# Optimization experiments

Hardware: AMD Instinct MI355X
Metric: run time of the kernel (lower is better)

## Reference

```python
import jax, jax.numpy as jnp
import numpy as np


def setup_inputs() -> dict:
    key = jax.random.key(0)
    k1, k2 = jax.random.split(key)
    B, C, H, W = 16, 512, 64, 64
    x_training = jax.random.normal(k1, (B, C, H, W), dtype=jnp.float32)
    x_pre = jax.random.normal(k2, (B, C, H, W), dtype=jnp.float32)
    return {"x_training": x_training, "x_pre": x_pre}


def reference(x_training, x_pre):
    B, C, H, W = x_training.shape
    q = x_pre.reshape(B, C, H * W)        # proj_query: B x C x N
    kv = x_training.reshape(B, C, H * W)  # proj_key/value: B x C x N
    # energy[b,c,d] = <q[b,c,:], kv[b,d,:]>  -> B x C x C
    energy = jnp.einsum('bcn,bdn->bcd', q, kv)
    # max-subtract trick (note: max - energy, not energy - max)
    energy_new = jnp.max(energy, axis=-1, keepdims=True) - energy
    attention = jax.nn.softmax(energy_new, axis=-1)  # B x C x C
    out = jnp.einsum('bcd,bdn->bcn', attention, kv).reshape(B, C, H, W)
    # final softmax over last (width) axis of the 4D map
    return jax.nn.softmax(out, axis=-1)
```

## Files before the change

### kernel.cpp

```cpp
#include <hip/hip_runtime.h>
#include <hip/hip_bf16.h>
#include <math.h>

#define CCH  512
#define NTOK 4096
#define NB   16
#define KSPL 2048
#define LDA  40

typedef __attribute__((ext_vector_type(8))) short s8v;
typedef __attribute__((ext_vector_type(4))) float f4v;
typedef unsigned short u16;

__device__ __forceinline__ void split2(float2 f, ushort2& hi, ushort2& lo) {
    __hip_bfloat162 h = __float22bfloat162_rn(f);
    float2 hf = __bfloat1622float2(h);
    __hip_bfloat162 l = __float22bfloat162_rn(make_float2(f.x - hf.x, f.y - hf.y));
    hi = *reinterpret_cast<ushort2*>(&h);
    lo = *reinterpret_cast<ushort2*>(&l);
}
__device__ __forceinline__ u16 bfrne(float x) {
    __hip_bfloat16 h = __float2bfloat16(x);
    return *reinterpret_cast<u16*>(&h);
}

__global__ __launch_bounds__(256, 2)
void energy_mfma(const float* __restrict__ q, const float* __restrict__ kv,
                 float* __restrict__ E) {
    __shared__ short Ah[128 * LDA], Al[128 * LDA], Bh[128 * LDA], Bl[128 * LDA];
    const int b  = blockIdx.z >> 1;
    const int s  = blockIdx.z & 1;
    const int c0 = blockIdx.y * 128, d0 = blockIdx.x * 128;
    const int tid  = threadIdx.x;
    const int lane = tid & 63, wave = tid >> 6;
    const int wm = wave & 1, wn = wave >> 1;
    const int l15 = lane & 15, quad = lane >> 4;

    const int srow = tid >> 1;
    const int skq  = (tid & 1) * 16;
    const float* ga = q  + ((size_t)(b * CCH + c0 + srow)) * NTOK + s * KSPL + skq;
    const float* gb = kv + ((size_t)(b * CCH + d0 + srow)) * NTOK + s * KSPL + skq;

    f4v acc[4][4];
#pragma unroll
    for (int i = 0; i < 4; ++i)
#pragma unroll
        for (int j = 0; j < 4; ++j) acc[i][j] = (f4v)0.f;

    float4 pa[4], pb[4];
#pragma unroll
    for (int i = 0; i < 4; ++i) {
        pa[i] = ((const float4*)ga)[i];
        pb[i] = ((const float4*)gb)[i];
    }

    for (int kc = 0; kc < KSPL; kc += 32) {
        __syncthreads();
#pragma unroll
        for (int i = 0; i < 4; ++i) {
            ushort2 h0, l0, h1, l1;
            split2(make_float2(pa[i].x, pa[i].y), h0, l0);
            split2(make_float2(pa[i].z, pa[i].w), h1, l1);
            *(ushort4*)&Ah[srow * LDA + skq + i * 4] = make_ushort4(h0.x, h0.y, h1.x, h1.y);
            *(ushort4*)&Al[srow * LDA + skq + i * 4] = make_ushort4(l0.x, l0.y, l1.x, l1.y);
            split2(make_float2(pb[i].x, pb[i].y), h0, l0);
            split2(make_float2(pb[i].z, pb[i].w), h1, l1);
            *(ushort4*)&Bh[srow * LDA + skq + i * 4] = make_ushort4(h0.x, h0.y, h1.x, h1.y);
            *(ushort4*)&Bl[srow * LDA + skq + i * 4] = make_ushort4(l0.x, l0.y, l1.x, l1.y);
        }
        __syncthreads();
        if (kc + 32 < KSPL) {
            const float* ga2 = ga + kc + 32;
            const float* gb2 = gb + kc + 32;
#pragma unroll
            for (int i = 0; i < 4; ++i) {
                pa[i] = ((const float4*)ga2)[i];
                pb[i] = ((const float4*)gb2)[i];
            }
        }
        const int koff = quad * 8;
        const int abase = (wm * 64 + l15) * LDA + koff;
        const int bbase = (wn * 64 + l15) * LDA + koff;
        s8v a_h[4], a_l[4];
#pragma unroll
        for (int i = 0; i < 4; ++i) {
            a_h[i] = *(const s8v*)&Ah[abase + i * 16 * LDA];
            a_l[i] = *(const s8v*)&Al[abase + i * 16 * LDA];
        }
#pragma unroll
        for (int j = 0; j < 4; ++j) {
            s8v b_h = *(const s8v*)&Bh[bbase + j * 16 * LDA];
            s8v b_l = *(const s8v*)&Bl[bbase + j * 16 * LDA];
#pragma unroll
            for (int i = 0; i < 4; ++i) {
                acc[i][j] = __builtin_amdgcn_mfma_f32_16x16x32_bf16(a_h[i], b_h, acc[i][j], 0, 0, 0);
                acc[i][j] = __builtin_amdgcn_mfma_f32_16x16x32_bf16(a_h[i], b_l, acc[i][j], 0, 0, 0);
                acc[i][j] = __builtin_amdgcn_mfma_f32_16x16x32_bf16(a_l[i], b_h, acc[i][j], 0, 0, 0);
            }
        }
    }

    float* Eb = E + ((size_t)(s * NB + b)) * CCH * CCH;
#pragma unroll
    for (int i = 0; i < 4; ++i)
#pragma unroll
        for (int r = 0; r < 4; ++r) {
            const int row = c0 + wm * 64 + i * 16 + quad * 4 + r;
#pragma unroll
            for (int j = 0; j < 4; ++j)
                Eb[(size_t)row * CCH + d0 + wn * 64 + j * 16 + l15] = acc[i][j][r];
        }
}

__global__ __launch_bounds__(256)
void attn_softmax(const float* __restrict__ E0, const float* __restrict__ E1,
                  u16* __restrict__ ah, u16* __restrict__ al) {
    __shared__ float red[4];
    const size_t base = (size_t)blockIdx.x * CCH;
    const int t = threadIdx.x;
    float e0 = E0[base + t] + E1[base + t];
    float e1 = E0[base + t + 256] + E1[base + t + 256];
    float m = fminf(e0, e1);
#pragma unroll
    for (int off = 32; off > 0; off >>= 1) m = fminf(m, __shfl_xor(m, off, 64));
    if ((t & 63) == 0) red[t >> 6] = m;
    __syncthreads();
    const float mAll = fminf(fminf(red[0], red[1]), fminf(red[2], red[3]));
    float x0 = __expf(mAll - e0);
    float x1 = __expf(mAll - e1);
    float sum = x0 + x1;
#pragma unroll
    for (int off = 32; off > 0; off >>= 1) sum += __shfl_xor(sum, off, 64);
    __syncthreads();
    if ((t & 63) == 0) red[t >> 6] = sum;
    __syncthreads();
    const float inv = 1.0f / (red[0] + red[1] + red[2] + red[3]);
    float a0 = x0 * inv, a1 = x1 * inv;
    __hip_bfloat16 h0 = __float2bfloat16(a0);
    __hip_bfloat16 h1 = __float2bfloat16(a1);
    ah[base + t]       = *reinterpret_cast<u16*>(&h0);
    ah[base + t + 256] = *reinterpret_cast<u16*>(&h1);
    __hip_bfloat16 g0 = __float2bfloat16(a0 - __bfloat162float(h0));
    __hip_bfloat16 g1 = __float2bfloat16(a1 - __bfloat162float(h1));
    al[base + t]       = *reinterpret_cast<u16*>(&g0);
    al[base + t + 256] = *reinterpret_cast<u16*>(&g1);
}

__global__ __launch_bounds__(256, 2)
void out_mfma(const u16* __restrict__ atth, const u16* __restrict__ attl,
              const float* __restrict__ kv, float* __restrict__ out) {
    __shared__ short Ah[128 * LDA], Al[128 * LDA], Bs[128 * LDA];
    const int b  = blockIdx.z;
    const int c0 = blockIdx.y * 128;
    const int n0 = blockIdx.x * 128;
    const int tid  = threadIdx.x;
    const int lane = tid & 63, wave = tid >> 6;
    const int wm = wave & 1, wn = wave >> 1;
    const int l15 = lane & 15, quad = lane >> 4;

    const int arow = tid >> 1, akq = (tid & 1) * 16;
    const u16* gah = atth + ((size_t)(b * CCH + c0 + arow)) * CCH + akq;
    const u16* gal = attl + ((size_t)(b * CCH + c0 + arow)) * CCH + akq;
    const int bn = tid & 127, bkg = (tid >> 7) * 16;
    const float* gb = kv + (size_t)b * CCH * NTOK + n0 + bn;

    f4v acc[4][4];
#pragma unroll
    for (int i = 0; i < 4; ++i)
#pragma unroll
        for (int j = 0; j < 4; ++j) acc[i][j] = (f4v)0.f;

    ushort4 pah[4], pal[4];
    float pbf[16];
#pragma unroll
    for (int i = 0; i < 4; ++i) {
        pah[i] = *(const ushort4*)(gah + i * 4);
        pal[i] = *(const ushort4*)(gal + i * 4);
    }
#pragma unroll
    for (int t = 0; t < 16; ++t) pbf[t] = gb[(size_t)(bkg + t) * NTOK];

    for (int kc = 0; kc < CCH; kc += 32) {
        __syncthreads();
#pragma unroll
        for (int i = 0; i < 4; ++i) {
            *(ushort4*)&Ah[arow * LDA + akq + i * 4] = pah[i];
            *(ushort4*)&Al[arow * LDA + akq + i * 4] = pal[i];
        }
#pragma unroll
        for (int p = 0; p < 4; ++p) {
            ushort4 v = make_ushort4(bfrne(pbf[p * 4 + 0]), bfrne(pbf[p * 4 + 1]),
                                     bfrne(pbf[p * 4 + 2]), bfrne(pbf[p * 4 + 3]));
            *(ushort4*)&Bs[bn * LDA + bkg + p * 4] = v;
        }
        __syncthreads();
        if (kc + 32 < CCH) {
#pragma unroll
            for (int i = 0; i < 4; ++i) {
                pah[i] = *(const ushort4*)(gah + kc + 32 + i * 4);
                pal[i] = *(const ushort4*)(gal + kc + 32 + i * 4);
            }
#pragma unroll
            for (int t = 0; t < 16; ++t) pbf[t] = gb[(size_t)(kc + 32 + bkg + t) * NTOK];
        }
        const int koff = quad * 8;
        const int abase = (wm * 64 + l15) * LDA + koff;
        const int bbase = (wn * 64 + l15) * LDA + koff;
        s8v a_h[4], a_l[4];
#pragma unroll
        for (int i = 0; i < 4; ++i) {
            a_h[i] = *(const s8v*)&Ah[abase + i * 16 * LDA];
            a_l[i] = *(const s8v*)&Al[abase + i * 16 * LDA];
        }
#pragma unroll
        for (int j = 0; j < 4; ++j) {
            s8v bb = *(const s8v*)&Bs[bbase + j * 16 * LDA];
#pragma unroll
            for (int i = 0; i < 4; ++i) {
                acc[i][j] = __builtin_amdgcn_mfma_f32_16x16x32_bf16(a_h[i], bb, acc[i][j], 0, 0, 0);
                acc[i][j] = __builtin_amdgcn_mfma_f32_16x16x32_bf16(a_l[i], bb, acc[i][j], 0, 0, 0);
            }
        }
    }

#pragma unroll
    for (int i = 0; i < 4; ++i) {
#pragma unroll
        for (int r = 0; r < 4; ++r) {
            float v0 = acc[i][0][r], v1 = acc[i][1][r], v2 = acc[i][2][r], v3 = acc[i][3][r];
            float m = fmaxf(fmaxf(v0, v1), fmaxf(v2, v3));
#pragma unroll
            for (int off = 8; off > 0; off >>= 1) m = fmaxf(m, __shfl_xor(m, off, 16));
            float e0 = __expf(v0 - m), e1 = __expf(v1 - m), e2 = __expf(v2 - m), e3 = __expf(v3 - m);
            float sum = e0 + e1 + e2 + e3;
#pragma unroll
            for (int off = 8; off > 0; off >>= 1) sum += __shfl_xor(sum, off, 16);
            const float inv = 1.0f / sum;
            const int row = c0 + wm * 64 + i * 16 + quad * 4 + r;
            float* op = out + ((size_t)(b * CCH + row)) * NTOK + n0 + wn * 64 + l15;
            op[0]  = e0 * inv;
            op[16] = e1 * inv;
            op[32] = e2 * inv;
            op[48] = e3 * inv;
        }
    }
}

extern "C" void kernel_launch(void* const* d_in, const int* in_sizes, int n_in,
                              void* d_out, int out_size, void* d_ws, size_t ws_size,
                              hipStream_t stream) {
    const float* x_training = (const float*)d_in[0];
    const float* x_pre      = (const float*)d_in[1];
    float* out = (float*)d_out;
    const size_t ES = (size_t)NB * CCH * CCH;
    float* E0 = (float*)d_ws;
    float* E1 = E0 + ES;
    u16* ath = (u16*)(E1 + ES);
    u16* atl = ath + ES;

    energy_mfma<<<dim3(4, 4, 32), 256, 0, stream>>>(x_pre, x_training, E0);
    attn_softmax<<<dim3(NB * CCH), 256, 0, stream>>>(E0, E1, ath, atl);
    out_mfma<<<dim3(NTOK / 128, CCH / 128, NB), 256, 0, stream>>>(ath, atl, x_training, out);
}
```

Measured before the change: 477.4 us.

## Switch split-bf16 MFMA to fp16 with fewer correction terms

Replaces the bf16 hi/lo split matmuls with fp16 MFMA. The energy GEMM now uses two products (A hi/lo times B hi only) instead of three. The output GEMM uses a single fp16 attention matrix instead of a hi/lo pair. This removes MFMA work, LDS traffic and the extra attention-matrix global traffic, and raises the occupancy hint to 3 blocks. The cost is lower accuracy: fp16 has a narrower range, which risks overflow or underflow, and dropping the correction terms leaves only about 11 bits of mantissa for B and the attention.

Result: faster. 450.4 us (-5.7%).

```diff
diff --git a/kernel.cpp b/kernel.cpp
--- a/kernel.cpp
+++ b/kernel.cpp
@@ -1,5 +1,4 @@
 #include <hip/hip_runtime.h>
-#include <hip/hip_bf16.h>
 #include <math.h>
 
 #define CCH  512
@@ -8,26 +7,26 @@
 #define KSPL 2048
 #define LDA  40
 
-typedef __attribute__((ext_vector_type(8))) short s8v;
+typedef __attribute__((ext_vector_type(8))) _Float16 h8v;
 typedef __attribute__((ext_vector_type(4))) float f4v;
 typedef unsigned short u16;
 
-__device__ __forceinline__ void split2(float2 f, ushort2& hi, ushort2& lo) {
-    __hip_bfloat162 h = __float22bfloat162_rn(f);
-    float2 hf = __bfloat1622float2(h);
-    __hip_bfloat162 l = __float22bfloat162_rn(make_float2(f.x - hf.x, f.y - hf.y));
-    hi = *reinterpret_cast<ushort2*>(&h);
-    lo = *reinterpret_cast<ushort2*>(&l);
-}
-__device__ __forceinline__ u16 bfrne(float x) {
-    __hip_bfloat16 h = __float2bfloat16(x);
-    return *reinterpret_cast<u16*>(&h);
-}
-
-__global__ __launch_bounds__(256, 2)
+__device__ __forceinline__ u16 f16bits(float x) {
+    _Float16 h = (_Float16)x;
+    return __builtin_bit_cast(u16, h);
+}
+__device__ __forceinline__ void splith(float x, u16& h, u16& l) {
+    _Float16 hh = (_Float16)x;
+    float hf = (float)hh;
+    _Float16 ll = (_Float16)(x - hf);
+    h = __builtin_bit_cast(u16, hh);
+    l = __builtin_bit_cast(u16, ll);
+}
+
+__global__ __launch_bounds__(256, 3)
 void energy_mfma(const float* __restrict__ q, const float* __restrict__ kv,
                  float* __restrict__ E) {
-    __shared__ short Ah[128 * LDA], Al[128 * LDA], Bh[128 * LDA], Bl[128 * LDA];
+    __shared__ short Ah[128 * LDA], Al[128 * LDA], Bh[128 * LDA];
     const int b  = blockIdx.z >> 1;
     const int s  = blockIdx.z & 1;
     const int c0 = blockIdx.y * 128, d0 = blockIdx.x * 128;
@@ -58,15 +57,16 @@
         __syncthreads();
 #pragma unroll
         for (int i = 0; i < 4; ++i) {
-            ushort2 h0, l0, h1, l1;
-            split2(make_float2(pa[i].x, pa[i].y), h0, l0);
-            split2(make_float2(pa[i].z, pa[i].w), h1, l1);
-            *(ushort4*)&Ah[srow * LDA + skq + i * 4] = make_ushort4(h0.x, h0.y, h1.x, h1.y);
-            *(ushort4*)&Al[srow * LDA + skq + i * 4] = make_ushort4(l0.x, l0.y, l1.x, l1.y);
-            split2(make_float2(pb[i].x, pb[i].y), h0, l0);
-            split2(make_float2(pb[i].z, pb[i].w), h1, l1);
-            *(ushort4*)&Bh[srow * LDA + skq + i * 4] = make_ushort4(h0.x, h0.y, h1.x, h1.y);
-            *(ushort4*)&Bl[srow * LDA + skq + i * 4] = make_ushort4(l0.x, l0.y, l1.x, l1.y);
+            u16 h0, l0, h1, l1, h2, l2, h3, l3;
+            splith(pa[i].x, h0, l0);
+            splith(pa[i].y, h1, l1);
+            splith(pa[i].z, h2, l2);
+            splith(pa[i].w, h3, l3);
+            *(ushort4*)&Ah[srow * LDA + skq + i * 4] = make_ushort4(h0, h1, h2, h3);
+            *(ushort4*)&Al[srow * LDA + skq + i * 4] = make_ushort4(l0, l1, l2, l3);
+            *(ushort4*)&Bh[srow * LDA + skq + i * 4] =
+                make_ushort4(f16bits(pb[i].x), f16bits(pb[i].y),
+                             f16bits(pb[i].z), f16bits(pb[i].w));
         }
         __syncthreads();
         if (kc + 32 < KSPL) {
@@ -81,21 +81,19 @@
         const int koff = quad * 8;
         const int abase = (wm * 64 + l15) * LDA + koff;
         const int bbase = (wn * 64 + l15) * LDA + koff;
-        s8v a_h[4], a_l[4];
+        h8v a_h[4], a_l[4];
 #pragma unroll
         for (int i = 0; i < 4; ++i) {
-            a_h[i] = *(const s8v*)&Ah[abase + i * 16 * LDA];
-            a_l[i] = *(const s8v*)&Al[abase + i * 16 * LDA];
+            a_h[i] = *(const h8v*)&Ah[abase + i * 16 * LDA];
+            a_l[i] = *(const h8v*)&Al[abase + i * 16 * LDA];
         }
 #pragma unroll
         for (int j = 0; j < 4; ++j) {
-            s8v b_h = *(const s8v*)&Bh[bbase + j * 16 * LDA];
-            s8v b_l = *(const s8v*)&Bl[bbase + j * 16 * LDA];
+            h8v b_h = *(const h8v*)&Bh[bbase + j * 16 * LDA];
 #pragma unroll
             for (int i = 0; i < 4; ++i) {
-                acc[i][j] = __builtin_amdgcn_mfma_f32_16x16x32_bf16(a_h[i], b_h, acc[i][j], 0, 0, 0);
-                acc[i][j] = __builtin_amdgcn_mfma_f32_16x16x32_bf16(a_h[i], b_l, acc[i][j], 0, 0, 0);
-                acc[i][j] = __builtin_amdgcn_mfma_f32_16x16x32_bf16(a_l[i], b_h, acc[i][j], 0, 0, 0);
+                acc[i][j] = __builtin_amdgcn_mfma_f32_16x16x32_f16(a_h[i], b_h, acc[i][j], 0, 0, 0);
+                acc[i][j] = __builtin_amdgcn_mfma_f32_16x16x32_f16(a_l[i], b_h, acc[i][j], 0, 0, 0);
             }
         }
     }
@@ -114,7 +112,7 @@
 
 __global__ __launch_bounds__(256)
 void attn_softmax(const float* __restrict__ E0, const float* __restrict__ E1,
-                  u16* __restrict__ ah, u16* __restrict__ al) {
+                  u16* __restrict__ ah) {
     __shared__ float red[4];
     const size_t base = (size_t)blockIdx.x * CCH;
     const int t = threadIdx.x;
@@ -135,21 +133,14 @@
     if ((t & 63) == 0) red[t >> 6] = sum;
     __syncthreads();
     const float inv = 1.0f / (red[0] + red[1] + red[2] + red[3]);
-    float a0 = x0 * inv, a1 = x1 * inv;
-    __hip_bfloat16 h0 = __float2bfloat16(a0);
-    __hip_bfloat16 h1 = __float2bfloat16(a1);
-    ah[base + t]       = *reinterpret_cast<u16*>(&h0);
-    ah[base + t + 256] = *reinterpret_cast<u16*>(&h1);
-    __hip_bfloat16 g0 = __float2bfloat16(a0 - __bfloat162float(h0));
-    __hip_bfloat16 g1 = __float2bfloat16(a1 - __bfloat162float(h1));
-    al[base + t]       = *reinterpret_cast<u16*>(&g0);
-    al[base + t + 256] = *reinterpret_cast<u16*>(&g1);
-}
-
-__global__ __launch_bounds__(256, 2)
-void out_mfma(const u16* __restrict__ atth, const u16* __restrict__ attl,
-              const float* __restrict__ kv, float* __restrict__ out) {
-    __shared__ short Ah[128 * LDA], Al[128 * LDA], Bs[128 * LDA];
+    ah[base + t]       = f16bits(x0 * inv);
+    ah[base + t + 256] = f16bits(x1 * inv);
+}
+
+__global__ __launch_bounds__(256, 3)
+void out_mfma(const u16* __restrict__ att, const float* __restrict__ kv,
+              float* __restrict__ out) {
+    __shared__ short Ah[128 * LDA], Bs[128 * LDA];
     const int b  = blockIdx.z;
     const int c0 = blockIdx.y * 128;
     const int n0 = blockIdx.x * 128;
@@ -159,8 +150,7 @@
     const int l15 = lane & 15, quad = lane >> 4;
 
     const int arow = tid >> 1, akq = (tid & 1) * 16;
-    const u16* gah = atth + ((size_t)(b * CCH + c0 + arow)) * CCH + akq;
-    const u16* gal = attl + ((size_t)(b * CCH + c0 + arow)) * CCH + akq;
+    const u16* gah = att + ((size_t)(b * CCH + c0 + arow)) * CCH + akq;
     const int bn = tid & 127, bkg = (tid >> 7) * 16;
     const float* gb = kv + (size_t)b * CCH * NTOK + n0 + bn;
 
@@ -170,56 +160,45 @@
 #pragma unroll
         for (int j = 0; j < 4; ++j) acc[i][j] = (f4v)0.f;
 
-    ushort4 pah[4], pal[4];
+    ushort4 pah[4];
     float pbf[16];
 #pragma unroll
-    for (int i = 0; i < 4; ++i) {
-        pah[i] = *(const ushort4*)(gah + i * 4);
-        pal[i] = *(const ushort4*)(gal + i * 4);
-    }
+    for (int i = 0; i < 4; ++i) pah[i] = *(const ushort4*)(gah + i * 4);
 #pragma unroll
     for (int t = 0; t < 16; ++t) pbf[t] = gb[(size_t)(bkg + t) * NTOK];
 
     for (int kc = 0; kc < CCH; kc += 32) {
         __syncthreads();
 #pragma unroll
-        for (int i = 0; i < 4; ++i) {
+        for (int i = 0; i < 4; ++i)
             *(ushort4*)&Ah[arow * LDA + akq + i * 4] = pah[i];
-            *(ushort4*)&Al[arow * LDA + akq + i * 4] = pal[i];
-        }
 #pragma unroll
         for (int p = 0; p < 4; ++p) {
-            ushort4 v = make_ushort4(bfrne(pbf[p * 4 + 0]), bfrne(pbf[p * 4 + 1]),
-                                     bfrne(pbf[p * 4 + 2]), bfrne(pbf[p * 4 + 3]));
+            ushort4 v = make_ushort4(f16bits(pbf[p * 4 + 0]), f16bits(pbf[p * 4 + 1]),
+                                     f16bits(pbf[p * 4 + 2]), f16bits(pbf[p * 4 + 3]));
             *(ushort4*)&Bs[bn * LDA + bkg + p * 4] = v;
         }
         __syncthreads();
         if (kc + 32 < CCH) {
 #pragma unroll
-            for (int i = 0; i < 4; ++i) {
+            for (int i = 0; i < 4; ++i)
                 pah[i] = *(const ushort4*)(gah + kc + 32 + i * 4);
-                pal[i] = *(const ushort4*)(gal + kc + 32 + i * 4);
-            }
 #pragma unroll
             for (int t = 0; t < 16; ++t) pbf[t] = gb[(size_t)(kc + 32 + bkg + t) * NTOK];
         }
         const int koff = quad * 8;
         const int abase = (wm * 64 + l15) * LDA + koff;
         const int bbase = (wn * 64 + l15) * LDA + koff;
-        s8v a_h[4], a_l[4];
-#pragma unroll
-        for (int i = 0; i < 4; ++i) {
-            a_h[i] = *(const s8v*)&Ah[abase + i * 16 * LDA];
-            a_l[i] = *(const s8v*)&Al[abase + i * 16 * LDA];
-        }
+        h8v a_h[4];
+#pragma unroll
+        for (int i = 0; i < 4; ++i)
+            a_h[i] = *(const h8v*)&Ah[abase + i * 16 * LDA];
 #pragma unroll
         for (int j = 0; j < 4; ++j) {
-            s8v bb = *(const s8v*)&Bs[bbase + j * 16 * LDA];
-#pragma unroll
-            for (int i = 0; i < 4; ++i) {
-                acc[i][j] = __builtin_amdgcn_mfma_f32_16x16x32_bf16(a_h[i], bb, acc[i][j], 0, 0, 0);
-                acc[i][j] = __builtin_amdgcn_mfma_f32_16x16x32_bf16(a_l[i], bb, acc[i][j], 0, 0, 0);
-            }
+            h8v bb = *(const h8v*)&Bs[bbase + j * 16 * LDA];
+#pragma unroll
+            for (int i = 0; i < 4; ++i)
+                acc[i][j] = __builtin_amdgcn_mfma_f32_16x16x32_f16(a_h[i], bb, acc[i][j], 0, 0, 0);
         }
     }
 
@@ -256,9 +235,8 @@
     float* E0 = (float*)d_ws;
     float* E1 = E0 + ES;
     u16* ath = (u16*)(E1 + ES);
-    u16* atl = ath + ES;
 
     energy_mfma<<<dim3(4, 4, 32), 256, 0, stream>>>(x_pre, x_training, E0);
-    attn_softmax<<<dim3(NB * CCH), 256, 0, stream>>>(E0, E1, ath, atl);
-    out_mfma<<<dim3(NTOK / 128, CCH / 128, NB), 256, 0, stream>>>(ath, atl, x_training, out);
-}
+    attn_softmax<<<dim3(NB * CCH), 256, 0, stream>>>(E0, E1, ath);
+    out_mfma<<<dim3(NTOK / 128, CCH / 128, NB), 256, 0, stream>>>(ath, x_training, out);
+}
```
